# Kernel tuning notes

Hardware: AMD Instinct MI355X
Metric: run time of the kernel (lower is better)

The kernel has to match this reference:

```python
import jax, jax.numpy as jnp
import numpy as np

B, S, D, H = 2, 2048, 1024, 16
DK = D // H  # 64


def setup_inputs() -> dict:
    key = jax.random.key(0)
    ks = jax.random.split(key, 9)
    s = 0.02
    return {
        "embeddings": jax.random.normal(ks[0], (B, S, D), jnp.float32),
        "Wq": jax.random.normal(ks[1], (H, D, DK), jnp.float32) * s,
        "bq": jax.random.normal(ks[2], (H, DK), jnp.float32) * s,
        "Wk": jax.random.normal(ks[3], (H, D, DK), jnp.float32) * s,
        "bk": jax.random.normal(ks[4], (H, DK), jnp.float32) * s,
        "Wv": jax.random.normal(ks[5], (H, D, DK), jnp.float32) * s,
        "bv": jax.random.normal(ks[6], (H, DK), jnp.float32) * s,
        "Wo": jax.random.normal(ks[7], (D, D), jnp.float32) * s,
        "bo": jax.random.normal(ks[8], (D,), jnp.float32) * s,
    }


def reference(embeddings, Wq, bq, Wk, bk, Wv, bv, Wo, bo):
    b, s, d = embeddings.shape
    dk = Wq.shape[-1]
    # batched per-head projections: [b,s,d] x [h,d,k] -> [b,h,s,k]
    q = jnp.einsum('bsd,hdk->bhsk', embeddings, Wq) + bq[None, :, None, :]
    k = jnp.einsum('bsd,hdk->bhsk', embeddings, Wk) + bk[None, :, None, :]
    v = jnp.einsum('bsd,hdk->bhsk', embeddings, Wv) + bv[None, :, None, :]
    scores = jnp.einsum('bhqk,bhsk->bhqs', q, k) / jnp.sqrt(jnp.float32(dk))
    causal_mask = jnp.triu(jnp.ones((s, s), dtype=bool), k=1)  # True above diagonal
    scores = jnp.where(causal_mask, jnp.float32(-1e9), scores)
    weights = jax.nn.softmax(scores, axis=-1)
    ctx = jnp.einsum('bhqs,bhsk->bhqk', weights, v)
    concat = ctx.transpose(0, 2, 1, 3).reshape(b, s, d)  # head-major concat, matches torch.cat
    return concat @ Wo + bo
```

## Files before the change

kernel.cpp:

```cpp
#include <hip/hip_runtime.h>
#include <hip/hip_bf16.h>

typedef unsigned short u16;
typedef unsigned int u32;
typedef __bf16 bf16x8 __attribute__((ext_vector_type(8)));
typedef float f32x4 __attribute__((ext_vector_type(4)));
typedef float f32x16 __attribute__((ext_vector_type(16)));

#define AS1 __attribute__((address_space(1)))
#define AS3 __attribute__((address_space(3)))

#define NB 2
#define NS 2048
#define ND 1024
#define NH 16
#define NK 64

__device__ __forceinline__ u16 f2bf(float f) {
  u32 u = __builtin_bit_cast(u32, f);
  return (u16)((u + 0x7FFFu + ((u >> 16) & 1u)) >> 16);
}

__device__ __forceinline__ u32 cvt_pk_bf16(float lo, float hi) {
  u32 u;
  asm("v_cvt_pk_bf16_f32 %0, %1, %2" : "=v"(u) : "v"(lo), "v"(hi));
  return u;
}

__device__ __forceinline__ void stage_tile(u16* lds, const u16* __restrict__ src, int rs,
                                           int wid, int lane) {
#pragma unroll
  for (int i = 0; i < 2; ++i) {
    int c = wid * 128 + i * 64 + lane;
    int row = c >> 3;
    int kc = (c & 7) ^ (row & 7);
    __builtin_amdgcn_global_load_lds((const AS1 u32*)(src + (size_t)row * rs + kc * 8),
                                     (AS3 u32*)(lds + (wid * 128 + i * 64) * 8), 16, 0, 0);
  }
}

__device__ __forceinline__ void stage_warp(u16* lds, const u16* __restrict__ src, int rs,
                                           int lane) {
#pragma unroll
  for (int i = 0; i < 8; ++i) {
    int c = i * 64 + lane;
    int row = c >> 3;
    int kc = (c & 7) ^ (row & 7);
    __builtin_amdgcn_global_load_lds((const AS1 u32*)(src + (size_t)row * rs + kc * 8),
                                     (AS3 u32*)(lds + i * 512), 16, 0, 0);
  }
}

__device__ __forceinline__ bf16x8 read_slot(const u16* lds, int row, int slot) {
  return *(const bf16x8*)(lds + row * 64 + (slot ^ (row & 7)) * 8);
}

__device__ __forceinline__ bf16x8 read_frag(const u16* lds, int row, int ks, int lane) {
  int slot = ((lane >> 4) + ks * 4) ^ (row & 7);
  return *(const bf16x8*)(lds + row * 64 + slot * 8);
}

__global__ __launch_bounds__(256) void convert_kernel(const float* __restrict__ src,
                                                      u16* __restrict__ dst, int n) {
  int i = (blockIdx.x * 256 + threadIdx.x) * 4;
  if (i >= n) return;
  float4 v = *(const float4*)(src + i);
  u32 w0 = cvt_pk_bf16(v.x, v.y);
  u32 w1 = cvt_pk_bf16(v.z, v.w);
  uint2 w; w.x = w0; w.y = w1;
  *(uint2*)(dst + i) = w;
}

__global__ __launch_bounds__(256) void transpose_conv(const float* __restrict__ src,
                                                      u16* __restrict__ dst, int R, int C) {
  __shared__ float tile[32][33];
  size_t base = (size_t)blockIdx.z * R * C;
  src += base;
  dst += base;
  int c0 = blockIdx.x * 32, r0 = blockIdx.y * 32;
  int tx = threadIdx.x, ty = threadIdx.y;
#pragma unroll
  for (int i = 0; i < 4; ++i)
    tile[ty + 8 * i][tx] = src[(size_t)(r0 + ty + 8 * i) * C + c0 + tx];
  __syncthreads();
#pragma unroll
  for (int i = 0; i < 4; ++i)
    dst[(size_t)(c0 + ty + 8 * i) * R + r0 + tx] = f2bf(tile[tx][ty + 8 * i]);
}

template <int MODE>
__global__ __launch_bounds__(256) void gemm128(const u16* __restrict__ A,
                                               const u16* __restrict__ Bt,
                                               const float* __restrict__ b0,
                                               const float* __restrict__ b1,
                                               const float* __restrict__ b2,
                                               u16* __restrict__ Qo, u16* __restrict__ Ko,
                                               u16* __restrict__ Vo,
                                               float* __restrict__ out) {
  __shared__ alignas(16) u16 lds_a[128 * 64];
  __shared__ alignas(16) u16 lds_b[128 * 64];
  int tid = threadIdx.x, lane = tid & 63, wid = tid >> 6;
  int wm = wid >> 1, wn = wid & 1;
  int m0 = blockIdx.x * 128, n0 = blockIdx.y * 128;
  int col = lane & 15;
  f32x4 zero4 = {0.f, 0.f, 0.f, 0.f};
  f32x4 acc[4][4];
#pragma unroll
  for (int i = 0; i < 4; ++i)
#pragma unroll
    for (int j = 0; j < 4; ++j) acc[i][j] = zero4;
  for (int k0 = 0; k0 < ND; k0 += 64) {
    stage_tile(lds_a, A + (size_t)m0 * ND + k0, ND, wid, lane);
    stage_tile(lds_a + 4096, A + (size_t)(m0 + 64) * ND + k0, ND, wid, lane);
    stage_tile(lds_b, Bt + (size_t)n0 * ND + k0, ND, wid, lane);
    stage_tile(lds_b + 4096, Bt + (size_t)(n0 + 64) * ND + k0, ND, wid, lane);
    __syncthreads();
#pragma unroll
    for (int ks = 0; ks < 2; ++ks) {
      bf16x8 af[4], bf[4];
#pragma unroll
      for (int i = 0; i < 4; ++i) af[i] = read_frag(lds_a, wm * 64 + i * 16 + col, ks, lane);
#pragma unroll
      for (int j = 0; j < 4; ++j) bf[j] = read_frag(lds_b, wn * 64 + j * 16 + col, ks, lane);
#pragma unroll
      for (int i = 0; i < 4; ++i)
#pragma unroll
        for (int j = 0; j < 4; ++j)
          acc[i][j] = __builtin_amdgcn_mfma_f32_16x16x32_bf16(af[i], bf[j], acc[i][j], 0, 0, 0);
    }
    __syncthreads();
  }
  int rbase = m0 + wm * 64 + (lane >> 4) * 4;
#pragma unroll
  for (int j = 0; j < 4; ++j) {
    int n = n0 + wn * 64 + j * 16 + col;
    if constexpr (MODE == 0) {
      int which = n >> 10, hh = (n >> 6) & 15, dk = n & 63;
      const float* bp = which == 0 ? b0 : which == 1 ? b1 : b2;
      float bn = bp[hh * 64 + dk];
      if (which == 0) {
#pragma unroll
        for (int i = 0; i < 4; ++i)
#pragma unroll
          for (int r = 0; r < 4; ++r) {
            int m = rbase + i * 16 + r;
            int bb = m >> 11, s = m & (NS - 1);
            Qo[((size_t)(bb * NH + hh) * NS + s) * NK + dk] =
                f2bf((acc[i][j][r] + bn) * 0.18033688f);
          }
      } else if (which == 1) {
#pragma unroll
        for (int i = 0; i < 4; ++i)
#pragma unroll
          for (int r = 0; r < 4; ++r) {
            int m = rbase + i * 16 + r;
            int bb = m >> 11, s = m & (NS - 1);
            Ko[((size_t)(bb * NH + hh) * NS + s) * NK + dk] = f2bf(acc[i][j][r] + bn);
          }
      } else {
#pragma unroll
        for (int i = 0; i < 4; ++i)
#pragma unroll
          for (int r = 0; r < 4; ++r) {
            int m = rbase + i * 16 + r;
            int bb = m >> 11, s = m & (NS - 1);
            int ss = (s & ~12) | ((s & 4) << 1) | ((s & 8) >> 1);
            Vo[((size_t)(bb * NH + hh) * NK + dk) * NS + ss] = f2bf(acc[i][j][r] + bn);
          }
      }
    } else {
      float bn = b0[n];
#pragma unroll
      for (int i = 0; i < 4; ++i)
#pragma unroll
        for (int r = 0; r < 4; ++r)
          out[(size_t)(rbase + i * 16 + r) * ND + n] = acc[i][j][r] + bn;
    }
  }
}

__global__ __launch_bounds__(64, 4) void attn_kernel(const u16* __restrict__ Q,
                                                     const u16* __restrict__ K,
                                                     const u16* __restrict__ Vt,
                                                     u16* __restrict__ ctx) {
  __shared__ alignas(16) u16 ldsK[2][4096];
  int lane = threadIdx.x & 63;
  int hi = lane >> 5, ln = lane & 31;
  int bh = blockIdx.x;
  int qt2 = 63 - (int)blockIdx.y;
  const u16* Qb = Q + bh * (NS * NK);
  const u16* Kb = K + bh * (NS * NK);
  const u16* Vb = Vt + bh * (NK * NS);
  int b = bh >> 4, h = bh & 15;
  u16* myK0 = &ldsK[0][0];
  u16* myK1 = &ldsK[1][0];

  int q0w = qt2 * 32;
  int qg = q0w + ln;
  bf16x8 qf[4];
#pragma unroll
  for (int ks = 0; ks < 4; ++ks)
    qf[ks] = *(const bf16x8*)(Qb + qg * NK + ks * 16 + hi * 8);

  f32x16 acc0, acc1;
#pragma unroll
  for (int r = 0; r < 16; ++r) { acc0[r] = 0.f; acc1[r] = 0.f; }
  float lp = 0.f;
  int tmask = qt2 >> 1;
  int nt = tmask + 1;

  stage_warp(myK0, Kb, NK, lane);
  if (nt > 1) stage_warp(myK1, Kb + 64 * NK, NK, lane);

#pragma unroll 1
  for (int t = 0; t < nt; ++t) {
    const u16* lk = (t & 1) ? myK1 : myK0;
    if (t + 1 < nt) {
      asm volatile("s_waitcnt vmcnt(8)" ::: "memory");
    } else {
      asm volatile("s_waitcnt vmcnt(0)" ::: "memory");
    }
    __builtin_amdgcn_sched_barrier(0);
    const u16* Vtb_ = Vb + t * 64;
    bf16x8 vf0[4], vf1[4];
#pragma unroll
    for (int ks = 0; ks < 4; ++ks) {
      vf0[ks] = *(const bf16x8*)(Vtb_ + (size_t)ln * NS + (2 * ks + hi) * 8);
      vf1[ks] = *(const bf16x8*)(Vtb_ + (size_t)(32 + ln) * NS + (2 * ks + hi) * 8);
    }
    f32x16 sc0, sc1;
#pragma unroll
    for (int r = 0; r < 16; ++r) { sc0[r] = 0.f; sc1[r] = 0.f; }
    __builtin_amdgcn_s_setprio(1);
#pragma unroll
    for (int ks = 0; ks < 4; ++ks) {
      bf16x8 kf0 = read_slot(lk, ln, 2 * ks + hi);
      sc0 = __builtin_amdgcn_mfma_f32_32x32x16_bf16(kf0, qf[ks], sc0, 0, 0, 0);
      bf16x8 kf1 = read_slot(lk, 32 + ln, 2 * ks + hi);
      sc1 = __builtin_amdgcn_mfma_f32_32x32x16_bf16(kf1, qf[ks], sc1, 0, 0, 0);
    }
    __builtin_amdgcn_s_setprio(0);
    if (t == tmask) {
#pragma unroll
      for (int r = 0; r < 16; ++r) {
        int kl = t * 64 + (r & 3) + 8 * (r >> 2) + 4 * hi;
        if (kl > qg) sc0[r] = -1e30f;
        if (kl + 32 > qg) sc1[r] = -1e30f;
      }
    }
    float ps[4] = {0.f, 0.f, 0.f, 0.f};
#pragma unroll
    for (int r = 0; r < 16; ++r) {
      float p = exp2f(sc0[r]);
      sc0[r] = p;
      ps[r & 3] += p;
    }
#pragma unroll
    for (int r = 0; r < 16; ++r) {
      float p = exp2f(sc1[r]);
      sc1[r] = p;
      ps[r & 3] += p;
    }
    lp += (ps[0] + ps[1]) + (ps[2] + ps[3]);
    u32 wd[8];
    bf16x8 pa[4];
#pragma unroll
    for (int i = 0; i < 8; ++i) wd[i] = cvt_pk_bf16(sc0[2 * i], sc0[2 * i + 1]);
    { uint4 q4; q4.x = wd[0]; q4.y = wd[1]; q4.z = wd[2]; q4.w = wd[3];
      pa[0] = __builtin_bit_cast(bf16x8, q4);
      q4.x = wd[4]; q4.y = wd[5]; q4.z = wd[6]; q4.w = wd[7];
      pa[1] = __builtin_bit_cast(bf16x8, q4); }
#pragma unroll
    for (int i = 0; i < 8; ++i) wd[i] = cvt_pk_bf16(sc1[2 * i], sc1[2 * i + 1]);
    { uint4 q4; q4.x = wd[0]; q4.y = wd[1]; q4.z = wd[2]; q4.w = wd[3];
      pa[2] = __builtin_bit_cast(bf16x8, q4);
      q4.x = wd[4]; q4.y = wd[5]; q4.z = wd[6]; q4.w = wd[7];
      pa[3] = __builtin_bit_cast(bf16x8, q4); }
    __builtin_amdgcn_s_setprio(1);
#pragma unroll
    for (int ks = 0; ks < 4; ++ks) {
      acc0 = __builtin_amdgcn_mfma_f32_32x32x16_bf16(pa[ks], vf0[ks], acc0, 0, 0, 0);
      acc1 = __builtin_amdgcn_mfma_f32_32x32x16_bf16(pa[ks], vf1[ks], acc1, 0, 0, 0);
    }
    __builtin_amdgcn_s_setprio(0);
    if (t + 2 < nt) {
      asm volatile("s_waitcnt lgkmcnt(0)" ::: "memory");
      __builtin_amdgcn_sched_barrier(0);
      stage_warp((t & 1) ? myK1 : myK0, Kb + (t + 2) * 64 * NK, NK, lane);
    }
  }
  lp += __shfl_xor(lp, 32);
  float inv = 1.0f / lp;
#pragma unroll
  for (int r = 0; r < 16; ++r) {
    int crow = (r & 3) + 8 * (r >> 2) + 4 * hi;
    float iv = __shfl(inv, crow);
    int qq = q0w + crow;
    size_t base = (size_t)(b * NS + qq) * ND + h * NK + ln;
    ctx[base] = f2bf(acc0[r] * iv);
    ctx[base + 32] = f2bf(acc1[r] * iv);
  }
}

extern "C" void kernel_launch(void* const* d_in, const int* in_sizes, int n_in,
                              void* d_out, int out_size, void* d_ws, size_t ws_size,
                              hipStream_t stream) {
  (void)in_sizes; (void)n_in; (void)out_size;
  const float* emb = (const float*)d_in[0];
  const float* Wq = (const float*)d_in[1];
  const float* bq = (const float*)d_in[2];
  const float* Wk = (const float*)d_in[3];
  const float* bk = (const float*)d_in[4];
  const float* Wv = (const float*)d_in[5];
  const float* bv = (const float*)d_in[6];
  const float* Wo = (const float*)d_in[7];
  const float* bo = (const float*)d_in[8];
  float* out = (float*)d_out;

  const size_t EMB_N = (size_t)NB * NS * ND;
  const size_t W_N = (size_t)NH * ND * NK;
  const size_t QKV_N = (size_t)NB * NH * NS * NK;
  if (ws_size < (EMB_N + 4 * W_N + 3 * QKV_N) * sizeof(u16)) return;
  u16* ws = (u16*)d_ws;
  u16* emb_bf = ws;
  u16* Wqt = emb_bf + EMB_N;
  u16* Wkt = Wqt + W_N;
  u16* Wvt = Wkt + W_N;
  u16* Wot = Wvt + W_N;
  u16* Qb = Wot + W_N;
  u16* Kb = Qb + QKV_N;
  u16* Vtb = Kb + QKV_N;
  u16* ctxb = emb_bf;

  convert_kernel<<<dim3((int)(EMB_N / 4 / 256)), dim3(256), 0, stream>>>(emb, emb_bf,
                                                                         (int)EMB_N);
  dim3 tb(32, 8);
  transpose_conv<<<dim3(2, 32, 16), tb, 0, stream>>>(Wq, Wqt, ND, NK);
  transpose_conv<<<dim3(2, 32, 16), tb, 0, stream>>>(Wk, Wkt, ND, NK);
  transpose_conv<<<dim3(2, 32, 16), tb, 0, stream>>>(Wv, Wvt, ND, NK);
  transpose_conv<<<dim3(32, 32, 1), tb, 0, stream>>>(Wo, Wot, ND, ND);
  gemm128<0><<<dim3(32, 24), dim3(256), 0, stream>>>(emb_bf, Wqt, bq, bk, bv, Qb, Kb, Vtb,
                                                     nullptr);
  attn_kernel<<<dim3(32, 64), dim3(64), 0, stream>>>(Qb, Kb, Vtb, ctxb);
  gemm128<1><<<dim3(32, 8), dim3(256), 0, stream>>>(ctxb, Wot, bo, nullptr, nullptr,
                                                    nullptr, nullptr, nullptr, out);
}
```

Measured before the change: 144.1 us.

## Load K into registers, compute row sums via MFMA, merge QKV weight transposes

The attention kernel drops its LDS double-buffered K staging. Each step now prefetches the next K tile straight into registers, ping-ponging between two register sets across a loop unrolled by two. The softmax denominator comes from an extra MFMA against a vector of bf16 ones instead of per-lane adds and a final shuffle, and launch bounds drop to 2 waves per SIMD to make room for the larger register footprint. The three Q/K/V weight transposes are merged into one launch to save launch overhead, at the cost of lower occupancy and more MFMA work per tile.

```diff
diff --git a/kernel.cpp b/kernel.cpp
--- a/kernel.cpp
+++ b/kernel.cpp
@@ -37,22 +37,6 @@
     __builtin_amdgcn_global_load_lds((const AS1 u32*)(src + (size_t)row * rs + kc * 8),
                                      (AS3 u32*)(lds + (wid * 128 + i * 64) * 8), 16, 0, 0);
   }
-}
-
-__device__ __forceinline__ void stage_warp(u16* lds, const u16* __restrict__ src, int rs,
-                                           int lane) {
-#pragma unroll
-  for (int i = 0; i < 8; ++i) {
-    int c = i * 64 + lane;
-    int row = c >> 3;
-    int kc = (c & 7) ^ (row & 7);
-    __builtin_amdgcn_global_load_lds((const AS1 u32*)(src + (size_t)row * rs + kc * 8),
-                                     (AS3 u32*)(lds + i * 512), 16, 0, 0);
-  }
-}
-
-__device__ __forceinline__ bf16x8 read_slot(const u16* lds, int row, int slot) {
-  return *(const bf16x8*)(lds + row * 64 + (slot ^ (row & 7)) * 8);
 }
 
 __device__ __forceinline__ bf16x8 read_frag(const u16* lds, int row, int ks, int lane) {
@@ -86,6 +70,26 @@
 #pragma unroll
   for (int i = 0; i < 4; ++i)
     dst[(size_t)(c0 + ty + 8 * i) * R + r0 + tx] = f2bf(tile[tx][ty + 8 * i]);
+}
+
+__global__ __launch_bounds__(256) void transpose_qkv(const float* __restrict__ Wq,
+                                                     const float* __restrict__ Wk,
+                                                     const float* __restrict__ Wv,
+                                                     u16* __restrict__ dst) {
+  __shared__ float tile[32][33];
+  int z = blockIdx.z;
+  int which = z >> 4, head = z & 15;
+  const float* src = (which == 0 ? Wq : which == 1 ? Wk : Wv) + (size_t)head * ND * NK;
+  u16* d = dst + (size_t)z * ND * NK;
+  int c0 = blockIdx.x * 32, r0 = blockIdx.y * 32;
+  int tx = threadIdx.x, ty = threadIdx.y;
+#pragma unroll
+  for (int i = 0; i < 4; ++i)
+    tile[ty + 8 * i][tx] = src[(size_t)(r0 + ty + 8 * i) * NK + c0 + tx];
+  __syncthreads();
+#pragma unroll
+  for (int i = 0; i < 4; ++i)
+    d[(size_t)(c0 + ty + 8 * i) * ND + r0 + tx] = f2bf(tile[tx][ty + 8 * i]);
 }
 
 template <int MODE>
@@ -179,11 +183,76 @@
   }
 }
 
-__global__ __launch_bounds__(64, 4) void attn_kernel(const u16* __restrict__ Q,
+__device__ __forceinline__ void attn_step(
+    int t, int nt, int tmask, int hi, int ln, int qg,
+    const u16* __restrict__ Kb, const u16* __restrict__ Vb,
+    const bf16x8 (&qf)[4], bf16x8 (&kT0)[4], bf16x8 (&kT1)[4], bf16x8 (&kN0)[4],
+    bf16x8 (&kN1)[4], f32x16& acc0, f32x16& acc1, f32x16& accL, bf16x8 ones) {
+  const u16* Vt_ = Vb + t * 64;
+  bf16x8 vf0[4], vf1[4];
+#pragma unroll
+  for (int ks = 0; ks < 4; ++ks) {
+    vf0[ks] = *(const bf16x8*)(Vt_ + (size_t)ln * NS + (2 * ks + hi) * 8);
+    vf1[ks] = *(const bf16x8*)(Vt_ + (size_t)(32 + ln) * NS + (2 * ks + hi) * 8);
+  }
+  if (t + 1 < nt) {
+    const u16* Kn_ = Kb + (size_t)(t + 1) * 64 * NK;
+#pragma unroll
+    for (int ks = 0; ks < 4; ++ks) {
+      kN0[ks] = *(const bf16x8*)(Kn_ + (size_t)ln * NK + ks * 16 + hi * 8);
+      kN1[ks] = *(const bf16x8*)(Kn_ + (size_t)(32 + ln) * NK + ks * 16 + hi * 8);
+    }
+  }
+  f32x16 sc0, sc1;
+#pragma unroll
+  for (int r = 0; r < 16; ++r) { sc0[r] = 0.f; sc1[r] = 0.f; }
+  __builtin_amdgcn_s_setprio(1);
+#pragma unroll
+  for (int ks = 0; ks < 4; ++ks) {
+    sc0 = __builtin_amdgcn_mfma_f32_32x32x16_bf16(kT0[ks], qf[ks], sc0, 0, 0, 0);
+    sc1 = __builtin_amdgcn_mfma_f32_32x32x16_bf16(kT1[ks], qf[ks], sc1, 0, 0, 0);
+  }
+  __builtin_amdgcn_s_setprio(0);
+  if (t == tmask) {
+#pragma unroll
+    for (int r = 0; r < 16; ++r) {
+      int kl = t * 64 + (r & 3) + 8 * (r >> 2) + 4 * hi;
+      if (kl > qg) sc0[r] = -1e30f;
+      if (kl + 32 > qg) sc1[r] = -1e30f;
+    }
+  }
+#pragma unroll
+  for (int r = 0; r < 16; ++r) sc0[r] = exp2f(sc0[r]);
+#pragma unroll
+  for (int r = 0; r < 16; ++r) sc1[r] = exp2f(sc1[r]);
+  u32 wd[8];
+  bf16x8 pa[4];
+#pragma unroll
+  for (int i = 0; i < 8; ++i) wd[i] = cvt_pk_bf16(sc0[2 * i], sc0[2 * i + 1]);
+  { uint4 q4; q4.x = wd[0]; q4.y = wd[1]; q4.z = wd[2]; q4.w = wd[3];
+    pa[0] = __builtin_bit_cast(bf16x8, q4);
+    q4.x = wd[4]; q4.y = wd[5]; q4.z = wd[6]; q4.w = wd[7];
+    pa[1] = __builtin_bit_cast(bf16x8, q4); }
+#pragma unroll
+  for (int i = 0; i < 8; ++i) wd[i] = cvt_pk_bf16(sc1[2 * i], sc1[2 * i + 1]);
+  { uint4 q4; q4.x = wd[0]; q4.y = wd[1]; q4.z = wd[2]; q4.w = wd[3];
+    pa[2] = __builtin_bit_cast(bf16x8, q4);
+    q4.x = wd[4]; q4.y = wd[5]; q4.z = wd[6]; q4.w = wd[7];
+    pa[3] = __builtin_bit_cast(bf16x8, q4); }
+  __builtin_amdgcn_s_setprio(1);
+#pragma unroll
+  for (int ks = 0; ks < 4; ++ks) {
+    acc0 = __builtin_amdgcn_mfma_f32_32x32x16_bf16(pa[ks], vf0[ks], acc0, 0, 0, 0);
+    acc1 = __builtin_amdgcn_mfma_f32_32x32x16_bf16(pa[ks], vf1[ks], acc1, 0, 0, 0);
+    accL = __builtin_amdgcn_mfma_f32_32x32x16_bf16(pa[ks], ones, accL, 0, 0, 0);
+  }
+  __builtin_amdgcn_s_setprio(0);
+}
+
+__global__ __launch_bounds__(64, 2) void attn_kernel(const u16* __restrict__ Q,
                                                      const u16* __restrict__ K,
                                                      const u16* __restrict__ Vt,
                                                      u16* __restrict__ ctx) {
-  __shared__ alignas(16) u16 ldsK[2][4096];
   int lane = threadIdx.x & 63;
   int hi = lane >> 5, ln = lane & 31;
   int bh = blockIdx.x;
@@ -192,8 +261,6 @@
   const u16* Kb = K + bh * (NS * NK);
   const u16* Vb = Vt + bh * (NK * NS);
   int b = bh >> 4, h = bh & 15;
-  u16* myK0 = &ldsK[0][0];
-  u16* myK1 = &ldsK[1][0];
 
   int q0w = qt2 * 32;
   int qg = q0w + ln;
@@ -202,99 +269,35 @@
   for (int ks = 0; ks < 4; ++ks)
     qf[ks] = *(const bf16x8*)(Qb + qg * NK + ks * 16 + hi * 8);
 
-  f32x16 acc0, acc1;
-#pragma unroll
-  for (int r = 0; r < 16; ++r) { acc0[r] = 0.f; acc1[r] = 0.f; }
-  float lp = 0.f;
+  u32 one2 = 0x3F803F80u;
+  uint4 o4; o4.x = one2; o4.y = one2; o4.z = one2; o4.w = one2;
+  bf16x8 ones = __builtin_bit_cast(bf16x8, o4);
+
+  f32x16 acc0, acc1, accL;
+#pragma unroll
+  for (int r = 0; r < 16; ++r) { acc0[r] = 0.f; acc1[r] = 0.f; accL[r] = 0.f; }
   int tmask = qt2 >> 1;
   int nt = tmask + 1;
 
-  stage_warp(myK0, Kb, NK, lane);
-  if (nt > 1) stage_warp(myK1, Kb + 64 * NK, NK, lane);
+  bf16x8 kA0[4], kA1[4], kB0[4], kB1[4];
+#pragma unroll
+  for (int ks = 0; ks < 4; ++ks) {
+    kA0[ks] = *(const bf16x8*)(Kb + (size_t)ln * NK + ks * 16 + hi * 8);
+    kA1[ks] = *(const bf16x8*)(Kb + (size_t)(32 + ln) * NK + ks * 16 + hi * 8);
+  }
 
 #pragma unroll 1
-  for (int t = 0; t < nt; ++t) {
-    const u16* lk = (t & 1) ? myK1 : myK0;
-    if (t + 1 < nt) {
-      asm volatile("s_waitcnt vmcnt(8)" ::: "memory");
-    } else {
-      asm volatile("s_waitcnt vmcnt(0)" ::: "memory");
-    }
-    __builtin_amdgcn_sched_barrier(0);
-    const u16* Vtb_ = Vb + t * 64;
-    bf16x8 vf0[4], vf1[4];
-#pragma unroll
-    for (int ks = 0; ks < 4; ++ks) {
-      vf0[ks] = *(const bf16x8*)(Vtb_ + (size_t)ln * NS + (2 * ks + hi) * 8);
-      vf1[ks] = *(const bf16x8*)(Vtb_ + (size_t)(32 + ln) * NS + (2 * ks + hi) * 8);
-    }
-    f32x16 sc0, sc1;
-#pragma unroll
-    for (int r = 0; r < 16; ++r) { sc0[r] = 0.f; sc1[r] = 0.f; }
-    __builtin_amdgcn_s_setprio(1);
-#pragma unroll
-    for (int ks = 0; ks < 4; ++ks) {
-      bf16x8 kf0 = read_slot(lk, ln, 2 * ks + hi);
-      sc0 = __builtin_amdgcn_mfma_f32_32x32x16_bf16(kf0, qf[ks], sc0, 0, 0, 0);
-      bf16x8 kf1 = read_slot(lk, 32 + ln, 2 * ks + hi);
-      sc1 = __builtin_amdgcn_mfma_f32_32x32x16_bf16(kf1, qf[ks], sc1, 0, 0, 0);
-    }
-    __builtin_amdgcn_s_setprio(0);
-    if (t == tmask) {
-#pragma unroll
-      for (int r = 0; r < 16; ++r) {
-        int kl = t * 64 + (r & 3) + 8 * (r >> 2) + 4 * hi;
-        if (kl > qg) sc0[r] = -1e30f;
-        if (kl + 32 > qg) sc1[r] = -1e30f;
-      }
-    }
-    float ps[4] = {0.f, 0.f, 0.f, 0.f};
-#pragma unroll
-    for (int r = 0; r < 16; ++r) {
-      float p = exp2f(sc0[r]);
-      sc0[r] = p;
-      ps[r & 3] += p;
-    }
-#pragma unroll
-    for (int r = 0; r < 16; ++r) {
-      float p = exp2f(sc1[r]);
-      sc1[r] = p;
-      ps[r & 3] += p;
-    }
-    lp += (ps[0] + ps[1]) + (ps[2] + ps[3]);
-    u32 wd[8];
-    bf16x8 pa[4];
-#pragma unroll
-    for (int i = 0; i < 8; ++i) wd[i] = cvt_pk_bf16(sc0[2 * i], sc0[2 * i + 1]);
-    { uint4 q4; q4.x = wd[0]; q4.y = wd[1]; q4.z = wd[2]; q4.w = wd[3];
-      pa[0] = __builtin_bit_cast(bf16x8, q4);
-      q4.x = wd[4]; q4.y = wd[5]; q4.z = wd[6]; q4.w = wd[7];
-      pa[1] = __builtin_bit_cast(bf16x8, q4); }
-#pragma unroll
-    for (int i = 0; i < 8; ++i) wd[i] = cvt_pk_bf16(sc1[2 * i], sc1[2 * i + 1]);
-    { uint4 q4; q4.x = wd[0]; q4.y = wd[1]; q4.z = wd[2]; q4.w = wd[3];
-      pa[2] = __builtin_bit_cast(bf16x8, q4);
-      q4.x = wd[4]; q4.y = wd[5]; q4.z = wd[6]; q4.w = wd[7];
-      pa[3] = __builtin_bit_cast(bf16x8, q4); }
-    __builtin_amdgcn_s_setprio(1);
-#pragma unroll
-    for (int ks = 0; ks < 4; ++ks) {
-      acc0 = __builtin_amdgcn_mfma_f32_32x32x16_bf16(pa[ks], vf0[ks], acc0, 0, 0, 0);
-      acc1 = __builtin_amdgcn_mfma_f32_32x32x16_bf16(pa[ks], vf1[ks], acc1, 0, 0, 0);
-    }
-    __builtin_amdgcn_s_setprio(0);
-    if (t + 2 < nt) {
-      asm volatile("s_waitcnt lgkmcnt(0)" ::: "memory");
-      __builtin_amdgcn_sched_barrier(0);
-      stage_warp((t & 1) ? myK1 : myK0, Kb + (t + 2) * 64 * NK, NK, lane);
-    }
-  }
-  lp += __shfl_xor(lp, 32);
-  float inv = 1.0f / lp;
+  for (int t = 0; t < nt; t += 2) {
+    attn_step(t, nt, tmask, hi, ln, qg, Kb, Vb, qf, kA0, kA1, kB0, kB1, acc0, acc1,
+              accL, ones);
+    if (t + 1 < nt)
+      attn_step(t + 1, nt, tmask, hi, ln, qg, Kb, Vb, qf, kB0, kB1, kA0, kA1, acc0,
+                acc1, accL, ones);
+  }
 #pragma unroll
   for (int r = 0; r < 16; ++r) {
     int crow = (r & 3) + 8 * (r >> 2) + 4 * hi;
-    float iv = __shfl(inv, crow);
+    float iv = 1.0f / accL[r];
     int qq = q0w + crow;
     size_t base = (size_t)(b * NS + qq) * ND + h * NK + ln;
     ctx[base] = f2bf(acc0[r] * iv);
@@ -324,9 +327,7 @@
   u16* ws = (u16*)d_ws;
   u16* emb_bf = ws;
   u16* Wqt = emb_bf + EMB_N;
-  u16* Wkt = Wqt + W_N;
-  u16* Wvt = Wkt + W_N;
-  u16* Wot = Wvt + W_N;
+  u16* Wot = Wqt + 3 * W_N;
   u16* Qb = Wot + W_N;
   u16* Kb = Qb + QKV_N;
   u16* Vtb = Kb + QKV_N;
@@ -335,9 +336,7 @@
   convert_kernel<<<dim3((int)(EMB_N / 4 / 256)), dim3(256), 0, stream>>>(emb, emb_bf,
                                                                          (int)EMB_N);
   dim3 tb(32, 8);
-  transpose_conv<<<dim3(2, 32, 16), tb, 0, stream>>>(Wq, Wqt, ND, NK);
-  transpose_conv<<<dim3(2, 32, 16), tb, 0, stream>>>(Wk, Wkt, ND, NK);
-  transpose_conv<<<dim3(2, 32, 16), tb, 0, stream>>>(Wv, Wvt, ND, NK);
+  transpose_qkv<<<dim3(2, 32, 48), tb, 0, stream>>>(Wq, Wk, Wv, Wqt);
   transpose_conv<<<dim3(32, 32, 1), tb, 0, stream>>>(Wo, Wot, ND, ND);
   gemm128<0><<<dim3(32, 24), dim3(256), 0, stream>>>(emb_bf, Wqt, bq, bk, bv, Qb, Kb, Vtb,
                                                      nullptr);
```

Measured after the change: 153.3 us. +6.4%, slower.
